# Performance work log

Hardware: AMD Instinct MI355X
Metric: run time of the kernel (lower is better)

The kernel has to match this reference:

```python
import jax, jax.numpy as jnp
import numpy as np

H = 768       # hidden size
NH = 12       # num attention heads
DH = H // NH  # head dim = 64
B = 32
S = 512


def setup_inputs() -> dict:
    key = jax.random.key(0)
    ks = jax.random.split(key, 7)
    scale = 1.0 / np.sqrt(H)
    return {
        "inputs": jax.random.normal(ks[0], (B, S, H), dtype=jnp.float32),
        "Wq": jax.random.normal(ks[1], (H, H), dtype=jnp.float32) * scale,
        "bq": jnp.zeros((H,), dtype=jnp.float32),
        "Wk": jax.random.normal(ks[2], (H, H), dtype=jnp.float32) * scale,
        "bk": jnp.zeros((H,), dtype=jnp.float32),
        "Wv": jax.random.normal(ks[3], (H, H), dtype=jnp.float32) * scale,
        "bv": jnp.zeros((H,), dtype=jnp.float32),
    }


def reference(inputs, Wq, bq, Wk, bk, Wv, bv):
    # BertSelfAttention: linear projections (torch Linear: x @ W.T + b)
    def split_heads(x):  # [B,S,H] -> [B,NH,S,DH]
        return x.reshape(B, S, NH, DH).transpose(0, 2, 1, 3)

    q = split_heads(inputs @ Wq.T + bq)
    k = split_heads(inputs @ Wk.T + bk)
    v = split_heads(inputs @ Wv.T + bv)

    # scores [B,NH,S,S]; the wrapper adds an all-zero attention mask (no-op)
    scores = jnp.einsum("bhqd,bhkd->bhqk", q, k) / jnp.sqrt(jnp.float32(DH))
    probs = jax.nn.softmax(scores, axis=-1)
    ctx = jnp.einsum("bhqk,bhkd->bhqd", probs, v)  # [B,NH,S,DH]
    ctx = ctx.transpose(0, 2, 1, 3).reshape(B, S, H)
    return jnp.tanh(ctx)
```

## Files before the change

### kernel.cpp

```cpp
#include <hip/hip_runtime.h>
#include <hip/hip_bf16.h>
#include <cmath>

#define Bc   32
#define Sc_  512
#define Hc   768
#define NHc  12
#define DHc  64
#define Mc   (Bc * Sc_)
#define Ntot (3 * Hc)

#define QSCALE 0.18033688011112042f

#define PANEL 196608

typedef __attribute__((ext_vector_type(8))) short short8v;
typedef __attribute__((ext_vector_type(8))) unsigned short ushort8v;
typedef __attribute__((ext_vector_type(4))) float f32x4;

static __device__ __forceinline__ ushort f2b(float f) {
    __hip_bfloat16 h = __float2bfloat16(f);
    return *reinterpret_cast<ushort*>(&h);
}
static __device__ __forceinline__ ushort2 f2b2(float a, float b) {
    __hip_bfloat162 h = __float22bfloat162_rn(float2{a, b});
    return *reinterpret_cast<ushort2*>(&h);
}

static __device__ __forceinline__ void gl2lds(const ushort* g, ushort* l) {
    __builtin_amdgcn_global_load_lds(
        (const __attribute__((address_space(1))) unsigned int*)g,
        (__attribute__((address_space(3))) unsigned int*)l, 16, 0, 0);
}

static __device__ __forceinline__ float fast_tanh(float x) {
    float e = __builtin_amdgcn_exp2f(x * 2.885390081777927f);
    return 1.0f - 2.0f * __builtin_amdgcn_rcpf(e + 1.0f);
}

__global__ __launch_bounds__(256) void convert_pack(
    const float* __restrict__ X,
    const float* __restrict__ Wq, const float* __restrict__ Wk,
    const float* __restrict__ Wv,
    const float* __restrict__ bq, const float* __restrict__ bk,
    const float* __restrict__ bv,
    ushort* __restrict__ Xt, ushort* __restrict__ Wt, float* __restrict__ bbp)
{
    const int bx = blockIdx.x;
    const int panel = bx / 12, kcg = bx % 12;
    const int t = threadIdx.x;

    __shared__ ushort T[128][68];

    const float* base;
    ushort* out;
    const bool isX = panel < 128;
    int nhalf = 0;
    if (isX) {
        base = X + (size_t)panel * 128 * Hc;
        out  = Xt + (size_t)(panel >> 1) * PANEL + (size_t)(panel & 1) * 8192;
    } else {
        int nblk = panel - 128;
        nhalf = nblk & 1;
        int n0 = nblk * 128;
        int z = n0 / Hc;
        int nn0 = n0 - z * Hc;
        const float* W = (z == 0) ? Wq : (z == 1) ? Wk : Wv;
        base = W + (size_t)nn0 * Hc;
        out  = Wt + (size_t)(nblk >> 1) * PANEL;
    }
    const int k0 = kcg * 64;

    const int slot = t & 15, rsub = t >> 4;
    #pragma unroll
    for (int rnd = 0; rnd < 8; ++rnd) {
        int row = rnd * 16 + rsub;
        const float* p = base + (size_t)row * Hc + k0 + slot * 4;
        float4 f = *(const float4*)p;
        ushort2 h0 = f2b2(f.x, f.y);
        ushort2 h1 = f2b2(f.z, f.w);
        ushort4 u;
        u.x = h0.x; u.y = h0.y; u.z = h1.x; u.w = h1.y;
        *(ushort4*)&T[row][slot * 4] = u;
    }
    __syncthreads();

    const int row_w = t & 127, khh = t >> 7;
    #pragma unroll
    for (int rnd = 0; rnd < 4; ++rnd) {
        int kc_l = rnd * 2 + khh;
        ushort4 lo = *(const ushort4*)&T[row_w][kc_l * 8];
        ushort4 hi = *(const ushort4*)&T[row_w][kc_l * 8 + 4];
        ushort8v o;
        o[0] = lo.x; o[1] = lo.y; o[2] = lo.z; o[3] = lo.w;
        o[4] = hi.x; o[5] = hi.y; o[6] = hi.z; o[7] = hi.w;
        size_t oidx;
        if (isX) {
            oidx = (size_t)kcg * 16384 + (size_t)row_w * 64
                 + (size_t)((kc_l ^ (row_w & 7)) << 3);
        } else {
            int n = nhalf * 128 + row_w;
            oidx = (size_t)kcg * 16384 + (size_t)(kc_l >> 2) * 8192
                 + (size_t)n * 32 + (size_t)((((kc_l & 3) ^ ((n >> 1) & 3)) << 3));
        }
        *(ushort8v*)&out[oidx] = o;
    }

    if (bx == 0) {
        for (int i = t; i < Ntot; i += 256) {
            int z2 = i / Hc, nn = i - z2 * Hc;
            bbp[i] = ((z2 == 0) ? bq : (z2 == 1) ? bk : bv)[nn];
        }
    }
}

static __device__ __forceinline__ void stage_slot(const ushort* g, ushort* l,
                                                  int wv, int lane) {
    const int c0 = wv * 1024;
    gl2lds(g + c0 + lane * 8,       l + c0);
    gl2lds(g + c0 + 512 + lane * 8, l + c0 + 512);
}

#define BAR    __builtin_amdgcn_s_barrier()
#define VMW(n) asm volatile("s_waitcnt vmcnt(" #n ")" ::: "memory")

#define PH_A_READS(kh) \
    _Pragma("unroll") \
    for (int mf = 0; mf < 8; ++mf) \
        a[mf] = *(const short8v*)&As[ab + mf * 1024 + ((((kh) * 4 + quad) ^ rs) << 3)];

#define PH_B_READS(kh, nq) \
    b0 = *(const short8v*)&Bs[bb + (kh) * 8192 + ((nq) * 2) * 512 + bswz]; \
    b1 = *(const short8v*)&Bs[bb + (kh) * 8192 + ((nq) * 2 + 1) * 512 + bswz];

#define PH_MFMA(nq) \
    __builtin_amdgcn_s_setprio(1); \
    _Pragma("unroll") \
    for (int mf = 0; mf < 8; ++mf) { \
        acc[mf][(nq) * 2]     = __builtin_amdgcn_mfma_f32_16x16x32_bf16( \
            a[mf], b0, acc[mf][(nq) * 2], 0, 0, 0); \
        acc[mf][(nq) * 2 + 1] = __builtin_amdgcn_mfma_f32_16x16x32_bf16( \
            a[mf], b1, acc[mf][(nq) * 2 + 1], 0, 0, 0); \
    } \
    __builtin_amdgcn_s_setprio(0);

__global__ __launch_bounds__(512, 2) void qkv_mfma(
    const ushort* __restrict__ Xt, const ushort* __restrict__ Wt,
    const float* __restrict__ bbp,
    ushort* __restrict__ Qb, ushort* __restrict__ Kt, ushort* __restrict__ Vt)
{
    __shared__ __align__(16) ushort As[32768];
    __shared__ __align__(16) ushort Bs[32768];

    const int tid = threadIdx.x;
    const int wv = tid >> 6, lane = tid & 63;
    const int quad = lane >> 4, l16 = lane & 15;
    const int wr = wv >> 2, wc = wv & 3;

    const int bid = blockIdx.x;
    const int swz = (bid & 7) * 72 + (bid >> 3);
    const int bx = swz / 9, by = swz % 9;

    const ushort* gA = Xt + (size_t)bx * PANEL;
    const ushort* gB = Wt + (size_t)by * PANEL;

    f32x4 acc[8][4];
    #pragma unroll
    for (int i = 0; i < 8; ++i)
        #pragma unroll
        for (int j = 0; j < 4; ++j) acc[i][j] = (f32x4)(0.f);

    const int rs   = l16 & 7;
    const int bswz = (quad ^ ((l16 >> 1) & 3)) << 3;
    const int arow = l16 * 64;
    const int brow = (wc * 64 + l16) * 32;

    short8v a[8], b0, b1;

    stage_slot(gA,        As,        wv, lane);
    stage_slot(gA + 8192, As + 8192, wv, lane);
    stage_slot(gB,        Bs,        wv, lane);
    stage_slot(gB + 8192, Bs + 8192, wv, lane);
    VMW(2);
    BAR;

    for (int kt = 0; kt < 11; ++kt) {
        const int cur = kt & 1;
        const ushort* gAn = gA + (size_t)(kt + 1) * 16384;
        const ushort* gBn = gB + (size_t)(kt + 1) * 16384;
        ushort* lAn = As + (cur ^ 1) * 16384;
        ushort* lBn = Bs + (cur ^ 1) * 16384;
        const int ab = cur * 16384 + wr * 8192 + arow;
        const int bb = cur * 16384 + brow;

        PH_A_READS(0)
        PH_B_READS(0, 0)
        stage_slot(gAn, lAn, wv, lane);
        BAR;
        PH_MFMA(0)
        BAR;

        PH_B_READS(0, 1)
        stage_slot(gAn + 8192, lAn + 8192, wv, lane);
        BAR;
        PH_MFMA(1)
        VMW(4);
        BAR;

        PH_A_READS(1)
        PH_B_READS(1, 0)
        stage_slot(gBn, lBn, wv, lane);
        BAR;
        PH_MFMA(0)
        BAR;

        PH_B_READS(1, 1)
        stage_slot(gBn + 8192, lBn + 8192, wv, lane);
        BAR;
        PH_MFMA(1)
        VMW(2);
        BAR;
    }

    {
        const int ab = 16384 + wr * 8192 + arow;
        const int bb = 16384 + brow;

        PH_A_READS(0)
        PH_B_READS(0, 0)
        BAR;
        PH_MFMA(0)
        BAR;

        PH_B_READS(0, 1)
        BAR;
        PH_MFMA(1)
        VMW(0);
        BAR;

        PH_A_READS(1)
        PH_B_READS(1, 0)
        BAR;
        PH_MFMA(0)
        BAR;

        PH_B_READS(1, 1)
        BAR;
        PH_MFMA(1)
    }

    const int z = by / 3;
    #pragma unroll
    for (int nf = 0; nf < 4; ++nf) {
        const int n  = by * 256 + wc * 64 + nf * 16 + l16;
        const int nn = n - z * Hc;
        const int h  = nn >> 6, d = nn & 63;
        const float bias = bbp[n];
        #pragma unroll
        for (int mf = 0; mf < 8; ++mf) {
            const int mbase = bx * 256 + wr * 128 + mf * 16 + quad * 4;
            const int bb2 = mbase >> 9;
            const int s0 = mbase & 511;
            const size_t head = (size_t)(bb2 * NHc + h) * (Sc_ * DHc);
            if (z == 0) {
                size_t basep = head + (size_t)s0 * DHc + d;
                #pragma unroll
                for (int r = 0; r < 4; ++r)
                    Qb[basep + (size_t)r * DHc] = f2b((acc[mf][nf][r] + bias) * QSCALE);
            } else if (z == 1) {
                size_t basep = head + (s0 >> 6) * 4096 + (d >> 3) * 512
                             + (s0 & 63) * 8 + (d & 7);
                #pragma unroll
                for (int r = 0; r < 4; ++r)
                    Kt[basep + r * 8] = f2b(acc[mf][nf][r] + bias);
            } else {
                size_t basep = head + (s0 >> 6) * 4096 + ((s0 & 63) >> 3) * 512
                             + d * 8 + (s0 & 7);
                ushort4 o;
                o.x = f2b(acc[mf][nf][0] + bias);
                o.y = f2b(acc[mf][nf][1] + bias);
                o.z = f2b(acc[mf][nf][2] + bias);
                o.w = f2b(acc[mf][nf][3] + bias);
                *(ushort4*)&Vt[basep] = o;
            }
        }
    }
}

__global__ __launch_bounds__(256, 2) void attn_mfma(
    const ushort* __restrict__ Qb, const ushort* __restrict__ Kt,
    const ushort* __restrict__ Vt, float* __restrict__ out)
{
    const int bid = blockIdx.x;
    const int super = bid >> 4, l = bid & 15;
    const int head_lin = super * 8 + (l & 7);
    const int qhalf = l >> 3;
    const int b = head_lin / NHc, h = head_lin % NHc;

    const int wave = threadIdx.x >> 6;
    const int lane = threadIdx.x & 63;
    const int quad = lane >> 4, l16 = lane & 15;
    const int q0 = qhalf * 256 + wave * 64;
    const int sw = l16 & 7;

    const size_t head = (size_t)head_lin * (Sc_ * DHc);
    const ushort* __restrict__ Q = Qb + head;
    const ushort* __restrict__ K = Kt + head;
    const ushort* __restrict__ V = Vt + head;

    __shared__ __align__(16) ushort Plds[4][1024];

    short8v aq[4][2];
    #pragma unroll
    for (int u = 0; u < 4; ++u)
        #pragma unroll
        for (int hf = 0; hf < 2; ++hf)
            aq[u][hf] = *(const short8v*)
                &Q[(size_t)(q0 + u * 16 + l16) * DHc + hf * 32 + quad * 8];

    short8v ones;
    #pragma unroll
    for (int i = 0; i < 8; ++i) ones[i] = (short)0x3F80;

    f32x4 o[4][4], rsum[4];
    #pragma unroll
    for (int u = 0; u < 4; ++u) {
        rsum[u] = (f32x4)(0.f);
        #pragma unroll
        for (int t = 0; t < 4; ++t) o[u][t] = (f32x4)(0.f);
    }

    for (int kb = 0; kb < 8; ++kb) {
        const ushort* Kb_ = K + kb * 4096;
        const ushort* Vb_ = V + kb * 4096;

        short8v kf[4][2], vf[4][2];
        #pragma unroll
        for (int t = 0; t < 4; ++t) {
            kf[t][0] = *(const short8v*)&Kb_[quad * 512 + (t * 16 + l16) * 8];
            kf[t][1] = *(const short8v*)&Kb_[(4 + quad) * 512 + (t * 16 + l16) * 8];
            vf[t][0] = *(const short8v*)&Vb_[quad * 512 + (t * 16 + l16) * 8];
            vf[t][1] = *(const short8v*)&Vb_[(4 + quad) * 512 + (t * 16 + l16) * 8];
        }

        #pragma unroll
        for (int u = 0; u < 4; ++u) {
            f32x4 sa[4];
            #pragma unroll
            for (int t = 0; t < 4; ++t) {
                f32x4 s = __builtin_amdgcn_mfma_f32_16x16x32_bf16(
                    kf[t][0], aq[u][0], (f32x4)(0.f), 0, 0, 0);
                sa[t] = __builtin_amdgcn_mfma_f32_16x16x32_bf16(
                    kf[t][1], aq[u][1], s, 0, 0, 0);
            }

            #pragma unroll
            for (int t = 0; t < 4; ++t) {
                float p0 = __builtin_amdgcn_exp2f(sa[t][0]);
                float p1 = __builtin_amdgcn_exp2f(sa[t][1]);
                float p2 = __builtin_amdgcn_exp2f(sa[t][2]);
                float p3 = __builtin_amdgcn_exp2f(sa[t][3]);
                ushort2 lo = f2b2(p0, p1);
                ushort2 hi = f2b2(p2, p3);
                ushort4 pk;
                pk.x = lo.x; pk.y = lo.y; pk.z = hi.x; pk.w = hi.y;
                int c = t * 2 + (quad >> 1);
                int addr = l16 * 64 + ((c ^ sw) * 8) + (quad & 1) * 4;
                *(ushort4*)&Plds[wave][addr] = pk;
            }

            short8v pa0 = *(const short8v*)&Plds[wave][l16 * 64 + ((quad ^ sw) * 8)];
            short8v pa1 = *(const short8v*)&Plds[wave][l16 * 64 + (((4 + quad) ^ sw) * 8)];

            rsum[u] = __builtin_amdgcn_mfma_f32_16x16x32_bf16(
                pa0, ones, rsum[u], 0, 0, 0);
            rsum[u] = __builtin_amdgcn_mfma_f32_16x16x32_bf16(
                pa1, ones, rsum[u], 0, 0, 0);

            #pragma unroll
            for (int t2 = 0; t2 < 4; ++t2) {
                o[u][t2] = __builtin_amdgcn_mfma_f32_16x16x32_bf16(
                    pa0, vf[t2][0], o[u][t2], 0, 0, 0);
                o[u][t2] = __builtin_amdgcn_mfma_f32_16x16x32_bf16(
                    pa1, vf[t2][1], o[u][t2], 0, 0, 0);
            }
        }
    }

    #pragma unroll
    for (int u = 0; u < 4; ++u) {
        #pragma unroll
        for (int r = 0; r < 4; ++r) {
            float inv = __builtin_amdgcn_rcpf(rsum[u][r]);
            int q = q0 + u * 16 + quad * 4 + r;
            size_t base = ((size_t)b * Sc_ + q) * Hc + h * DHc;
            #pragma unroll
            for (int t2 = 0; t2 < 4; ++t2)
                out[base + t2 * 16 + l16] = fast_tanh(o[u][t2][r] * inv);
        }
    }
}

extern "C" void kernel_launch(void* const* d_in, const int* in_sizes, int n_in,
                              void* d_out, int out_size, void* d_ws, size_t ws_size,
                              hipStream_t stream) {
    const float* X  = (const float*)d_in[0];
    const float* Wq = (const float*)d_in[1];
    const float* bq = (const float*)d_in[2];
    const float* Wk = (const float*)d_in[3];
    const float* bk = (const float*)d_in[4];
    const float* Wv = (const float*)d_in[5];
    const float* bv = (const float*)d_in[6];
    float* out = (float*)d_out;

    ushort* Qb  = (ushort*)d_ws;
    ushort* Kt  = Qb + (size_t)Mc * Hc;
    ushort* Vt  = Kt + (size_t)Mc * Hc;
    ushort* Xt  = Vt + (size_t)Mc * Hc;
    ushort* Wt  = Xt + (size_t)Mc * Hc;
    float*  bbp = (float*)(Wt + (size_t)Ntot * Hc);

    convert_pack<<<dim3(1752), 256, 0, stream>>>(
        X, Wq, Wk, Wv, bq, bk, bv, Xt, Wt, bbp);

    qkv_mfma<<<dim3(576), 512, 0, stream>>>(Xt, Wt, bbp, Qb, Kt, Vt);

    attn_mfma<<<dim3(768), 256, 0, stream>>>(Qb, Kt, Vt, out);
}
```

Measured before the change: 241.4 us.

## Unify X and W packed layouts into k-half split panels and reorder staging

Changes the packed bf16 layout of X to match the W layout (k split into two 32-wide halves, 32-element rows with a shared XOR swizzle). The pack kernel now writes contiguous 16-byte chunks per row with the swizzle applied on the LDS read side. The GEMM LDS reads use the same offset formula for A and B. The staging order is changed so each k-half of A and B arrives together, letting the first half's compute start after a looser vmcnt wait. This aims at cheaper address math, more coalesced pack writes and better load/compute overlap, but the wait-count bookkeeping must match the new issue order.

Result: faster. 226.1 us (-6.4%).

```diff
diff --git a/kernel.cpp b/kernel.cpp
--- a/kernel.cpp
+++ b/kernel.cpp
@@ -54,14 +54,14 @@
 
     const float* base;
     ushort* out;
-    const bool isX = panel < 128;
-    int nhalf = 0;
-    if (isX) {
+    int half128;
+    if (panel < 128) {
         base = X + (size_t)panel * 128 * Hc;
-        out  = Xt + (size_t)(panel >> 1) * PANEL + (size_t)(panel & 1) * 8192;
+        out  = Xt + (size_t)(panel >> 1) * PANEL;
+        half128 = panel & 1;
     } else {
         int nblk = panel - 128;
-        nhalf = nblk & 1;
+        half128 = nblk & 1;
         int n0 = nblk * 128;
         int z = n0 / Hc;
         int nn0 = n0 - z * Hc;
@@ -85,25 +85,21 @@
     }
     __syncthreads();
 
-    const int row_w = t & 127, khh = t >> 7;
+    const int gslot = t & 3, rowl = t >> 2;
     #pragma unroll
     for (int rnd = 0; rnd < 4; ++rnd) {
-        int kc_l = rnd * 2 + khh;
+        const int kh = rnd >> 1;
+        const int row_w = (rnd & 1) * 64 + rowl;
+        const int rowg = half128 * 128 + row_w;
+        const int g = gslot ^ ((rowg >> 1) & 3);
+        const int kc_l = kh * 4 + g;
         ushort4 lo = *(const ushort4*)&T[row_w][kc_l * 8];
         ushort4 hi = *(const ushort4*)&T[row_w][kc_l * 8 + 4];
         ushort8v o;
         o[0] = lo.x; o[1] = lo.y; o[2] = lo.z; o[3] = lo.w;
         o[4] = hi.x; o[5] = hi.y; o[6] = hi.z; o[7] = hi.w;
-        size_t oidx;
-        if (isX) {
-            oidx = (size_t)kcg * 16384 + (size_t)row_w * 64
-                 + (size_t)((kc_l ^ (row_w & 7)) << 3);
-        } else {
-            int n = nhalf * 128 + row_w;
-            oidx = (size_t)kcg * 16384 + (size_t)(kc_l >> 2) * 8192
-                 + (size_t)n * 32 + (size_t)((((kc_l & 3) ^ ((n >> 1) & 3)) << 3));
-        }
-        *(ushort8v*)&out[oidx] = o;
+        *(ushort8v*)&out[(size_t)kcg * 16384 + (size_t)kh * 8192
+                         + (size_t)rowg * 32 + gslot * 8] = o;
     }
 
     if (bx == 0) {
@@ -127,11 +123,11 @@
 #define PH_A_READS(kh) \
     _Pragma("unroll") \
     for (int mf = 0; mf < 8; ++mf) \
-        a[mf] = *(const short8v*)&As[ab + mf * 1024 + ((((kh) * 4 + quad) ^ rs) << 3)];
+        a[mf] = *(const short8v*)&As[cbase + (kh) * 8192 + mf * 512 + aoff];
 
 #define PH_B_READS(kh, nq) \
-    b0 = *(const short8v*)&Bs[bb + (kh) * 8192 + ((nq) * 2) * 512 + bswz]; \
-    b1 = *(const short8v*)&Bs[bb + (kh) * 8192 + ((nq) * 2 + 1) * 512 + bswz];
+    b0 = *(const short8v*)&Bs[cbase + (kh) * 8192 + (nq) * 1024 + boff]; \
+    b1 = *(const short8v*)&Bs[cbase + (kh) * 8192 + (nq) * 1024 + 512 + boff];
 
 #define PH_MFMA(nq) \
     __builtin_amdgcn_s_setprio(1); \
@@ -170,18 +166,17 @@
         #pragma unroll
         for (int j = 0; j < 4; ++j) acc[i][j] = (f32x4)(0.f);
 
-    const int rs   = l16 & 7;
-    const int bswz = (quad ^ ((l16 >> 1) & 3)) << 3;
-    const int arow = l16 * 64;
-    const int brow = (wc * 64 + l16) * 32;
+    const int aswz = ((quad ^ ((l16 >> 1) & 3)) << 3);
+    const int aoff = (wr * 128 + l16) * 32 + aswz;
+    const int boff = (wc * 64 + l16) * 32 + aswz;
 
     short8v a[8], b0, b1;
 
     stage_slot(gA,        As,        wv, lane);
+    stage_slot(gB,        Bs,        wv, lane);
     stage_slot(gA + 8192, As + 8192, wv, lane);
-    stage_slot(gB,        Bs,        wv, lane);
     stage_slot(gB + 8192, Bs + 8192, wv, lane);
-    VMW(2);
+    VMW(4);
     BAR;
 
     for (int kt = 0; kt < 11; ++kt) {
@@ -190,8 +185,7 @@
         const ushort* gBn = gB + (size_t)(kt + 1) * 16384;
         ushort* lAn = As + (cur ^ 1) * 16384;
         ushort* lBn = Bs + (cur ^ 1) * 16384;
-        const int ab = cur * 16384 + wr * 8192 + arow;
-        const int bb = cur * 16384 + brow;
+        const int cbase = cur * 16384;
 
         PH_A_READS(0)
         PH_B_READS(0, 0)
@@ -201,7 +195,7 @@
         BAR;
 
         PH_B_READS(0, 1)
-        stage_slot(gAn + 8192, lAn + 8192, wv, lane);
+        stage_slot(gBn, lBn, wv, lane);
         BAR;
         PH_MFMA(1)
         VMW(4);
@@ -209,7 +203,7 @@
 
         PH_A_READS(1)
         PH_B_READS(1, 0)
-        stage_slot(gBn, lBn, wv, lane);
+        stage_slot(gAn + 8192, lAn + 8192, wv, lane);
         BAR;
         PH_MFMA(0)
         BAR;
@@ -218,13 +212,12 @@
         stage_slot(gBn + 8192, lBn + 8192, wv, lane);
         BAR;
         PH_MFMA(1)
-        VMW(2);
+        VMW(4);
         BAR;
     }
 
     {
-        const int ab = 16384 + wr * 8192 + arow;
-        const int bb = 16384 + brow;
+        const int cbase = 16384;
 
         PH_A_READS(0)
         PH_B_READS(0, 0)
```
